# Kernel tuning notes

Measured on AMD Instinct MI355X. Metric: run time of the kernel, lower is better.

## Reference

```python
import jax, jax.numpy as jnp
import numpy as np

QUERY_DIM = 1024
KEY_DIM = 768
NUM_HEADS = 16
HEAD_DIM = QUERY_DIM // NUM_HEADS
SCALE = HEAD_DIM ** -0.5


def setup_inputs() -> dict:
    key = jax.random.key(0)
    ks = jax.random.split(key, 11)
    B, Nq, Nk = 4, 4096, 1024
    s_q = QUERY_DIM ** -0.5
    s_k = KEY_DIM ** -0.5
    return {
        "query": jax.random.normal(ks[0], (B, Nq, QUERY_DIM), jnp.float32),
        "key": jax.random.normal(ks[1], (B, Nk, KEY_DIM), jnp.float32),
        "value": jax.random.normal(ks[2], (B, Nk, KEY_DIM), jnp.float32),
        "Wq": jax.random.normal(ks[3], (QUERY_DIM, QUERY_DIM), jnp.float32) * s_q,
        "bq": jnp.zeros((QUERY_DIM,), jnp.float32),
        "Wk": jax.random.normal(ks[4], (KEY_DIM, QUERY_DIM), jnp.float32) * s_k,
        "bk": jnp.zeros((QUERY_DIM,), jnp.float32),
        "Wv": jax.random.normal(ks[5], (KEY_DIM, QUERY_DIM), jnp.float32) * s_k,
        "bv": jnp.zeros((QUERY_DIM,), jnp.float32),
        "Wo": jax.random.normal(ks[6], (QUERY_DIM, QUERY_DIM), jnp.float32) * s_q,
        "bo": jnp.zeros((QUERY_DIM,), jnp.float32),
    }


def reference(query, key, value, Wq, bq, Wk, bk, Wv, bv, Wo, bo):
    B, Nq, _ = query.shape
    Nk = key.shape[1]
    # projections to (B, H, N, d)
    q = (query @ Wq + bq).reshape(B, Nq, NUM_HEADS, HEAD_DIM).transpose(0, 2, 1, 3)
    k = (key @ Wk + bk).reshape(B, Nk, NUM_HEADS, HEAD_DIM).transpose(0, 2, 1, 3)
    v = (value @ Wv + bv).reshape(B, Nk, NUM_HEADS, HEAD_DIM).transpose(0, 2, 1, 3)
    attn = jnp.einsum("bhqd,bhkd->bhqk", q, k) * SCALE
    attn = jax.nn.softmax(attn, axis=-1)
    out = jnp.einsum("bhqk,bhkd->bhqd", attn, v)
    out = out.transpose(0, 2, 1, 3).reshape(B, Nq, QUERY_DIM)
    return out @ Wo + bo
```

## Files before the change

kernel.cpp:

```cpp
#include <hip/hip_runtime.h>
#include <hip/hip_bf16.h>
#include <stdint.h>


typedef unsigned short u16;
typedef __attribute__((ext_vector_type(8))) short short8;
typedef __attribute__((ext_vector_type(4))) float f32x4;

#define B_SZ 4
#define NQ   4096
#define NK   1024
#define QDIM 1024
#define KDIM 768
#define NH   16
#define HD   64
#define QSCALE (0.125f * 1.44269504f)

__device__ __forceinline__ u16 f2bf(float f) {
  union { float f; uint32_t u; } v; v.f = f;
  uint32_t u = v.u;
  return (u16)((u + 0x7FFFu + ((u >> 16) & 1u)) >> 16);
}

__device__ __forceinline__ uint32_t pk2(float a, float b) {
  union { __hip_bfloat162 h; uint32_t u; } cv;
  cv.h = __float22bfloat162_rn(float2{a, b});
  return cv.u;
}

__device__ __forceinline__ float fexp2(float x) {
  return __builtin_amdgcn_exp2f(x);
}

__device__ __forceinline__ void async16(u16* lds, const u16* g) {
  __builtin_amdgcn_global_load_lds(
      (__attribute__((address_space(1))) void*)(g),
      (__attribute__((address_space(3))) void*)(lds), 16, 0, 0);
}

__global__ __launch_bounds__(256) void f32_to_bf16_all(const float* __restrict__ q,
                                                       const float* __restrict__ k,
                                                       const float* __restrict__ v,
                                                       u16* __restrict__ oq,
                                                       u16* __restrict__ ok,
                                                       u16* __restrict__ ov,
                                                       int n4q, int n4kv) {
  int i = blockIdx.x * 256 + threadIdx.x;
  const float* in; u16* out; int idx;
  if (i < n4q) { in = q; out = oq; idx = i; }
  else if (i < n4q + n4kv) { in = k; out = ok; idx = i - n4q; }
  else if (i < n4q + 2 * n4kv) { in = v; out = ov; idx = i - n4q - n4kv; }
  else return;
  f32x4 vv = ((const f32x4*)in)[idx];
  uint2 o = {pk2(vv.x, vv.y), pk2(vv.z, vv.w)};
  ((uint2*)out)[idx] = o;
}

__global__ __launch_bounds__(256) void transpose4_k(const float* __restrict__ W0,
                                                    const float* __restrict__ W1,
                                                    const float* __restrict__ W2,
                                                    const float* __restrict__ W3,
                                                    u16* __restrict__ T0,
                                                    u16* __restrict__ T1,
                                                    u16* __restrict__ T2,
                                                    u16* __restrict__ T3) {
  const int z = blockIdx.z;
  const float* W = (z == 0) ? W0 : (z == 1) ? W1 : (z == 2) ? W2 : W3;
  u16* T = (z == 0) ? T0 : (z == 1) ? T1 : (z == 2) ? T2 : T3;
  const int K = (z == 1 || z == 2) ? KDIM : QDIM;
  const int N = QDIM;
  int nb = blockIdx.x * 32, kb = blockIdx.y * 32;
  if (kb >= K) return;
  __shared__ float t[32][33];
  int tx = threadIdx.x & 31, ty = threadIdx.x >> 5;
#pragma unroll
  for (int i = 0; i < 4; ++i)
    t[ty + i * 8][tx] = W[(size_t)(kb + ty + i * 8) * N + nb + tx];
  __syncthreads();
#pragma unroll
  for (int i = 0; i < 4; ++i)
    T[(size_t)(nb + ty + i * 8) * K + kb + tx] = f2bf(t[tx][ty + i * 8]);
}

__global__ __launch_bounds__(512, 2) void gemm_bt256(const u16* __restrict__ A,
                                                     const u16* __restrict__ Bt,
                                                     const float* __restrict__ bias,
                                                     float* __restrict__ Cf,
                                                     u16* __restrict__ Cb,
                                                     int M, int N, int K,
                                                     int out_bf16, float scale) {
  __shared__ __align__(16) u16 Al[3][128 * 64];
  __shared__ __align__(16) u16 Bl[3][256 * 64];
  const int tid = threadIdx.x;
  const int w = tid >> 6, lane = tid & 63;
  const int g = lane >> 4, l15 = lane & 15;
  const int sw = l15 & 7;
  const int bid = blockIdx.x;
  const int cpx = gridDim.x >> 3;
  const int swz = (bid & 7) * cpx + (bid >> 3);
  const int nby = N >> 8;
  const int mbase = (swz / nby) * 128, nbase = (swz % nby) * 256;
  const int wm = (w & 1) * 64, wn = (w >> 1) * 64;
  const int NT = K >> 6;

  const int ca0 = 0 * 512 + tid, ca1 = 1 * 512 + tid;
  const int ra0 = ca0 >> 3, rc0 = ((ca0 & 7) ^ (ra0 & 7)) * 8;
  const int ra1 = ca1 >> 3, rc1 = ((ca1 & 7) ^ (ra1 & 7)) * 8;
  const u16* pa0 = A + (size_t)(mbase + ra0) * K + rc0;
  const u16* pa1 = A + (size_t)(mbase + ra1) * K + rc1;
  const u16* pb[4];
#pragma unroll
  for (int i = 0; i < 4; ++i) {
    int c = i * 512 + tid;
    int row = c >> 3, col = ((c & 7) ^ (row & 7)) * 8;
    pb[i] = Bt + (size_t)(nbase + row) * K + col;
  }
  const int lA0 = (0 * 512 + w * 64) * 8, lA1 = (1 * 512 + w * 64) * 8;
  int lB[4];
#pragma unroll
  for (int i = 0; i < 4; ++i) lB[i] = (i * 512 + w * 64) * 8;

  f32x4 zero4 = {0.f, 0.f, 0.f, 0.f};
  f32x4 acc[4][4];
#pragma unroll
  for (int i = 0; i < 4; ++i)
#pragma unroll
    for (int j = 0; j < 4; ++j) acc[i][j] = zero4;

  async16(&Al[0][lA0], pa0); async16(&Al[0][lA1], pa1);
#pragma unroll
  for (int i = 0; i < 4; ++i) async16(&Bl[0][lB[i]], pb[i]);
  pa0 += 64; pa1 += 64;
#pragma unroll
  for (int i = 0; i < 4; ++i) pb[i] += 64;
  async16(&Al[1][lA0], pa0); async16(&Al[1][lA1], pa1);
#pragma unroll
  for (int i = 0; i < 4; ++i) async16(&Bl[1][lB[i]], pb[i]);
  pa0 += 64; pa1 += 64;
#pragma unroll
  for (int i = 0; i < 4; ++i) pb[i] += 64;
  asm volatile("s_waitcnt vmcnt(6)" ::: "memory");
  __builtin_amdgcn_sched_barrier(0);
  __builtin_amdgcn_s_barrier();

  int cb = 0, sb = 2;
  for (int kt = 0; kt < NT; ++kt) {
    const u16* Ap = &Al[cb][0];
    const u16* Bp = &Bl[cb][0];
    const bool st = (kt + 2 < NT);

    short8 af[4][2], bfa[2][2];
#pragma unroll
    for (int mt = 0; mt < 4; ++mt) {
      af[mt][0] = *(const short8*)&Ap[(wm + mt * 16 + l15) * 64 + (g ^ sw) * 8];
      af[mt][1] = *(const short8*)&Ap[(wm + mt * 16 + l15) * 64 + ((4 + g) ^ sw) * 8];
    }
#pragma unroll
    for (int nt = 0; nt < 2; ++nt) {
      bfa[nt][0] = *(const short8*)&Bp[(wn + nt * 16 + l15) * 64 + (g ^ sw) * 8];
      bfa[nt][1] = *(const short8*)&Bp[(wn + nt * 16 + l15) * 64 + ((4 + g) ^ sw) * 8];
    }
    if (st) {
      async16(&Al[sb][lA0], pa0);
      async16(&Al[sb][lA1], pa1);
      async16(&Bl[sb][lB[0]], pb[0]);
      async16(&Bl[sb][lB[1]], pb[1]);
    }
    __builtin_amdgcn_s_barrier();
    asm volatile("s_waitcnt lgkmcnt(0)" ::: "memory");
    __builtin_amdgcn_sched_barrier(0);
    __builtin_amdgcn_s_setprio(1);
#pragma unroll
    for (int ks = 0; ks < 2; ++ks)
#pragma unroll
      for (int mt = 0; mt < 4; ++mt)
#pragma unroll
        for (int nt = 0; nt < 2; ++nt)
          acc[mt][nt] = __builtin_amdgcn_mfma_f32_16x16x32_bf16(af[mt][ks], bfa[nt][ks],
                                                                acc[mt][nt], 0, 0, 0);
    __builtin_amdgcn_s_setprio(0);
    __builtin_amdgcn_s_barrier();

    short8 bfb[2][2];
#pragma unroll
    for (int nt = 0; nt < 2; ++nt) {
      bfb[nt][0] = *(const short8*)&Bp[(wn + (nt + 2) * 16 + l15) * 64 + (g ^ sw) * 8];
      bfb[nt][1] = *(const short8*)&Bp[(wn + (nt + 2) * 16 + l15) * 64 + ((4 + g) ^ sw) * 8];
    }
    if (st) {
      async16(&Bl[sb][lB[2]], pb[2]);
      async16(&Bl[sb][lB[3]], pb[3]);
      pa0 += 64; pa1 += 64;
#pragma unroll
      for (int i = 0; i < 4; ++i) pb[i] += 64;
    }
    __builtin_amdgcn_s_barrier();
    asm volatile("s_waitcnt lgkmcnt(0)" ::: "memory");
    __builtin_amdgcn_sched_barrier(0);
    __builtin_amdgcn_s_setprio(1);
#pragma unroll
    for (int ks = 0; ks < 2; ++ks)
#pragma unroll
      for (int mt = 0; mt < 4; ++mt)
#pragma unroll
        for (int nt = 0; nt < 2; ++nt)
          acc[mt][nt + 2] = __builtin_amdgcn_mfma_f32_16x16x32_bf16(af[mt][ks], bfb[nt][ks],
                                                                    acc[mt][nt + 2], 0, 0, 0);
    __builtin_amdgcn_s_setprio(0);

    if (kt < NT - 2) {
      asm volatile("s_waitcnt vmcnt(6)" ::: "memory");
    } else if (kt == NT - 2) {
      asm volatile("s_waitcnt vmcnt(0)" ::: "memory");
    }
    __builtin_amdgcn_sched_barrier(0);
    __builtin_amdgcn_s_barrier();
    cb = (cb == 2) ? 0 : cb + 1;
    sb = (sb == 2) ? 0 : sb + 1;
  }

#pragma unroll
  for (int nt = 0; nt < 4; ++nt) {
    int col = nbase + wn + nt * 16 + l15;
    float bv = bias[col];
#pragma unroll
    for (int mt = 0; mt < 4; ++mt)
#pragma unroll
      for (int r = 0; r < 4; ++r) {
        int row = mbase + wm + mt * 16 + g * 4 + r;
        float v = (acc[mt][nt][r] + bv) * scale;
        if (out_bf16) Cb[(size_t)row * N + col] = f2bf(v);
        else          Cf[(size_t)row * N + col] = v;
      }
  }
}

__global__ __launch_bounds__(256) void gemm_kv(const u16* __restrict__ kA,
                                               const u16* __restrict__ vA,
                                               const u16* __restrict__ Wk,
                                               const u16* __restrict__ Wv,
                                               const float* __restrict__ bk,
                                               const float* __restrict__ bv,
                                               u16* __restrict__ Kp,
                                               u16* __restrict__ VT,
                                               int M, int N, int K) {
  __shared__ __align__(16) u16 Al[128 * 64];
  __shared__ __align__(16) u16 Bl[128 * 64];
  const int bid = blockIdx.x;
  const int swz = (bid & 7) * 64 + (bid >> 3);
  const int ct = swz >> 8;
  const int mbase = (swz & 31) * 128, nbase = ((swz >> 5) & 7) * 128;
  const u16* A  = ct ? vA : kA;
  const u16* Bt = ct ? Wv : Wk;
  const float* bias = ct ? bv : bk;
  const int tid = threadIdx.x;
  const int w = tid >> 6, lane = tid & 63;
  const int g = lane >> 4, l15 = lane & 15;
  const int sw = l15 & 7;
  const int wm = (w & 1) * 64, wn = (w >> 1) * 64;

  f32x4 zero4 = {0.f, 0.f, 0.f, 0.f};
  f32x4 acc[4][4];
#pragma unroll
  for (int i = 0; i < 4; ++i)
#pragma unroll
    for (int j = 0; j < 4; ++j) acc[i][j] = zero4;

  for (int kb = 0; kb < K; kb += 64) {
#pragma unroll
    for (int i = 0; i < 4; ++i) {
      int cbase = w * 256 + i * 64;
      int c = cbase + lane;
      int row = c >> 3;
      int kc8 = ((c & 7) ^ (row & 7)) * 8;
      async16(&Al[cbase * 8], A + (size_t)(mbase + row) * K + kb + kc8);
      async16(&Bl[cbase * 8], Bt + (size_t)(nbase + row) * K + kb + kc8);
    }
    __syncthreads();
#pragma unroll
    for (int ks = 0; ks < 2; ++ks) {
      short8 af[4], bf[4];
#pragma unroll
      for (int mt = 0; mt < 4; ++mt)
        af[mt] = *(const short8*)&Al[(wm + mt * 16 + l15) * 64 + ((ks * 4 + g) ^ sw) * 8];
#pragma unroll
      for (int nt = 0; nt < 4; ++nt)
        bf[nt] = *(const short8*)&Bl[(wn + nt * 16 + l15) * 64 + ((ks * 4 + g) ^ sw) * 8];
      if (ct) {
#pragma unroll
        for (int nt = 0; nt < 4; ++nt)
#pragma unroll
          for (int mt = 0; mt < 4; ++mt)
            acc[nt][mt] = __builtin_amdgcn_mfma_f32_16x16x32_bf16(bf[nt], af[mt],
                                                                  acc[nt][mt], 0, 0, 0);
      } else {
#pragma unroll
        for (int mt = 0; mt < 4; ++mt)
#pragma unroll
          for (int nt = 0; nt < 4; ++nt)
            acc[mt][nt] = __builtin_amdgcn_mfma_f32_16x16x32_bf16(af[mt], bf[nt],
                                                                  acc[mt][nt], 0, 0, 0);
      }
    }
    __syncthreads();
  }

  if (ct) {
#pragma unroll
    for (int mt = 0; mt < 4; ++mt) {
      int m = mbase + wm + mt * 16 + l15;
#pragma unroll
      for (int nt = 0; nt < 4; ++nt)
#pragma unroll
        for (int r = 0; r < 4; ++r) {
          int n = nbase + wn + nt * 16 + g * 4 + r;
          VT[(size_t)n * M + m] = f2bf(acc[nt][mt][r] + bias[n]);
        }
    }
  } else {
#pragma unroll
    for (int nt = 0; nt < 4; ++nt) {
      int col = nbase + wn + nt * 16 + l15;
      float bvv = bias[col];
#pragma unroll
      for (int mt = 0; mt < 4; ++mt)
#pragma unroll
        for (int r = 0; r < 4; ++r) {
          int row = mbase + wm + mt * 16 + g * 4 + r;
          Kp[(size_t)row * N + col] = f2bf(acc[mt][nt][r] + bvv);
        }
    }
  }
}

__global__ __launch_bounds__(256, 2) void attn_kernel(const u16* __restrict__ Qp,
                                                      const u16* __restrict__ Kp,
                                                      const u16* __restrict__ VT,
                                                      u16* __restrict__ AO) {
  __shared__ __align__(16) u16 K_lds[2][64 * 64];
  __shared__ __align__(16) u16 V_lds[3][64 * 64];
  __shared__ __align__(16) u16 P_lds[4][32 * 64];

  const int tid = threadIdx.x;
  const int w = tid >> 6, lane = tid & 63;
  const int g = lane >> 4, l15 = lane & 15;
  const int sw = l15 & 7;
  const int bh = blockIdx.y, b = bh >> 4, h = bh & 15;
  const int qrow0 = blockIdx.x * 128 + w * 32;
  const int MT = B_SZ * NK;

  const int cbase0 = (w * 2 + 0) * 64;
  const int cbase1 = (w * 2 + 1) * 64;
  const int c0 = cbase0 + lane, c1 = cbase1 + lane;
  const int row0 = c0 >> 3, kc80 = ((c0 & 7) ^ (row0 & 7)) * 8;
  const int row1 = c1 >> 3, kc81 = ((c1 & 7) ^ (row1 & 7)) * 8;

  const u16* kp0 = Kp + (size_t)(b * NK + row0) * QDIM + h * HD + kc80;
  const u16* kp1 = Kp + (size_t)(b * NK + row1) * QDIM + h * HD + kc81;
  const u16* vp0 = VT + (size_t)(h * HD + row0) * MT + b * NK + kc80;
  const u16* vp1 = VT + (size_t)(h * HD + row1) * MT + b * NK + kc81;

  const int rb = l15 * 64;
  const int cs0 = (g ^ sw) * 8;
  const int cs1 = ((4 + g) ^ sw) * 8;
  const int pwb = rb + (((g >> 1) ^ (sw & 1)) * 8) + (g & 1) * 4;
  const int pms = sw & 6;

  short8 ones8;
#pragma unroll
  for (int j = 0; j < 8; ++j) ones8[j] = (short)0x3F80;

  short8 qf[2][2];
#pragma unroll
  for (int qt = 0; qt < 2; ++qt)
#pragma unroll
    for (int ks = 0; ks < 2; ++ks) {
      size_t row = (size_t)(b * NQ + qrow0 + qt * 16 + l15);
      qf[qt][ks] = *(const short8*)(Qp + row * QDIM + h * HD + ks * 32 + g * 8);
    }

  f32x4 zero4 = {0.f, 0.f, 0.f, 0.f};
  f32x4 o4[4][2];
  f32x4 lacc[2];
#pragma unroll
  for (int dt = 0; dt < 4; ++dt)
#pragma unroll
    for (int qt = 0; qt < 2; ++qt) o4[dt][qt] = zero4;
  lacc[0] = zero4; lacc[1] = zero4;

  u16* Pl = &P_lds[w][0];

  async16(&K_lds[0][cbase0 * 8], kp0);
  async16(&K_lds[0][cbase1 * 8], kp1);
  async16(&V_lds[0][cbase0 * 8], vp0);
  async16(&V_lds[0][cbase1 * 8], vp1);
  kp0 += 64 * QDIM; kp1 += 64 * QDIM; vp0 += 64; vp1 += 64;
  __syncthreads();

  async16(&K_lds[1][cbase0 * 8], kp0);
  async16(&K_lds[1][cbase1 * 8], kp1);
  async16(&V_lds[1][cbase0 * 8], vp0);
  async16(&V_lds[1][cbase1 * 8], vp1);
  kp0 += 64 * QDIM; kp1 += 64 * QDIM; vp0 += 64; vp1 += 64;

  {
    const u16* Kl = &K_lds[0][0];
    f32x4 sc[4][2];
    short8 kf0[4], kf1[4];
#pragma unroll
    for (int mt = 0; mt < 4; ++mt) {
      kf0[mt] = *(const short8*)&Kl[mt * 1024 + rb + cs0];
      kf1[mt] = *(const short8*)&Kl[mt * 1024 + rb + cs1];
    }
    __builtin_amdgcn_s_setprio(1);
#pragma unroll
    for (int mt = 0; mt < 4; ++mt)
#pragma unroll
      for (int qt = 0; qt < 2; ++qt)
        sc[mt][qt] = __builtin_amdgcn_mfma_f32_16x16x32_bf16(kf0[mt], qf[qt][0],
                                                             zero4, 0, 0, 0);
#pragma unroll
    for (int mt = 0; mt < 4; ++mt)
#pragma unroll
      for (int qt = 0; qt < 2; ++qt)
        sc[mt][qt] = __builtin_amdgcn_mfma_f32_16x16x32_bf16(kf1[mt], qf[qt][1],
                                                             sc[mt][qt], 0, 0, 0);
    __builtin_amdgcn_s_setprio(0);
#pragma unroll
    for (int qt = 0; qt < 2; ++qt)
#pragma unroll
      for (int mt = 0; mt < 4; ++mt) {
        float p0 = fexp2(sc[mt][qt][0]);
        float p1 = fexp2(sc[mt][qt][1]);
        float p2 = fexp2(sc[mt][qt][2]);
        float p3 = fexp2(sc[mt][qt][3]);
        uint2 pk = {pk2(p0, p1), pk2(p2, p3)};
        *(uint2*)&Pl[qt * 1024 + pwb + ((mt * 2) ^ pms) * 8] = pk;
      }
  }
  __syncthreads();

  for (int kc = 1; kc < NK / 64; ++kc) {
    const int pv = (kc - 1) % 3;
    if (kc + 1 < NK / 64) {
      const int nk = (kc + 1) & 1, nv = (kc + 1) % 3;
      async16(&K_lds[nk][cbase0 * 8], kp0);
      async16(&K_lds[nk][cbase1 * 8], kp1);
      async16(&V_lds[nv][cbase0 * 8], vp0);
      async16(&V_lds[nv][cbase1 * 8], vp1);
      kp0 += 64 * QDIM; kp1 += 64 * QDIM; vp0 += 64; vp1 += 64;
    }
    const u16* Kl = &K_lds[kc & 1][0];
    const u16* Vl = &V_lds[pv][0];

    short8 pb[2][2], vf[2][4], kf[2][4];
#pragma unroll
    for (int qt = 0; qt < 2; ++qt) {
      pb[0][qt] = *(const short8*)&Pl[qt * 1024 + rb + cs0];
      pb[1][qt] = *(const short8*)&Pl[qt * 1024 + rb + cs1];
    }
#pragma unroll
    for (int dt = 0; dt < 4; ++dt) {
      vf[0][dt] = *(const short8*)&Vl[dt * 1024 + rb + cs0];
      vf[1][dt] = *(const short8*)&Vl[dt * 1024 + rb + cs1];
    }
#pragma unroll
    for (int mt = 0; mt < 4; ++mt) {
      kf[0][mt] = *(const short8*)&Kl[mt * 1024 + rb + cs0];
      kf[1][mt] = *(const short8*)&Kl[mt * 1024 + rb + cs1];
    }

    f32x4 sc[4][2];
    __builtin_amdgcn_s_setprio(1);
#pragma unroll
    for (int mt = 0; mt < 4; ++mt)
#pragma unroll
      for (int qt = 0; qt < 2; ++qt)
        sc[mt][qt] = __builtin_amdgcn_mfma_f32_16x16x32_bf16(kf[0][mt], qf[qt][0],
                                                             zero4, 0, 0, 0);
#pragma unroll
    for (int qt = 0; qt < 2; ++qt)
      lacc[qt] = __builtin_amdgcn_mfma_f32_16x16x32_bf16(ones8, pb[0][qt],
                                                         lacc[qt], 0, 0, 0);
#pragma unroll
    for (int dt = 0; dt < 4; ++dt)
#pragma unroll
      for (int qt = 0; qt < 2; ++qt)
        o4[dt][qt] = __builtin_amdgcn_mfma_f32_16x16x32_bf16(vf[0][dt], pb[0][qt],
                                                             o4[dt][qt], 0, 0, 0);
#pragma unroll
    for (int mt = 0; mt < 4; ++mt)
#pragma unroll
      for (int qt = 0; qt < 2; ++qt)
        sc[mt][qt] = __builtin_amdgcn_mfma_f32_16x16x32_bf16(kf[1][mt], qf[qt][1],
                                                             sc[mt][qt], 0, 0, 0);
#pragma unroll
    for (int qt = 0; qt < 2; ++qt)
      lacc[qt] = __builtin_amdgcn_mfma_f32_16x16x32_bf16(ones8, pb[1][qt],
                                                         lacc[qt], 0, 0, 0);
#pragma unroll
    for (int dt = 0; dt < 4; ++dt)
#pragma unroll
      for (int qt = 0; qt < 2; ++qt)
        o4[dt][qt] = __builtin_amdgcn_mfma_f32_16x16x32_bf16(vf[1][dt], pb[1][qt],
                                                             o4[dt][qt], 0, 0, 0);
    __builtin_amdgcn_s_setprio(0);

#pragma unroll
    for (int qt = 0; qt < 2; ++qt)
#pragma unroll
      for (int mt = 0; mt < 4; ++mt) {
        float p0 = fexp2(sc[mt][qt][0]);
        float p1 = fexp2(sc[mt][qt][1]);
        float p2 = fexp2(sc[mt][qt][2]);
        float p3 = fexp2(sc[mt][qt][3]);
        uint2 pk = {pk2(p0, p1), pk2(p2, p3)};
        *(uint2*)&Pl[qt * 1024 + pwb + ((mt * 2) ^ pms) * 8] = pk;
      }

    asm volatile("s_waitcnt vmcnt(2)" ::: "memory");
    __builtin_amdgcn_sched_barrier(0);
    __builtin_amdgcn_s_barrier();
  }

  asm volatile("s_waitcnt vmcnt(0)" ::: "memory");
  __builtin_amdgcn_sched_barrier(0);
  __builtin_amdgcn_s_barrier();

  {
    const u16* Vl = &V_lds[(NK / 64 - 1) % 3][0];
    short8 pb[2][2], vf[2][4];
#pragma unroll
    for (int qt = 0; qt < 2; ++qt) {
      pb[0][qt] = *(const short8*)&Pl[qt * 1024 + rb + cs0];
      pb[1][qt] = *(const short8*)&Pl[qt * 1024 + rb + cs1];
    }
#pragma unroll
    for (int dt = 0; dt < 4; ++dt) {
      vf[0][dt] = *(const short8*)&Vl[dt * 1024 + rb + cs0];
      vf[1][dt] = *(const short8*)&Vl[dt * 1024 + rb + cs1];
    }
    __builtin_amdgcn_s_setprio(1);
#pragma unroll
    for (int ks = 0; ks < 2; ++ks) {
#pragma unroll
      for (int qt = 0; qt < 2; ++qt)
        lacc[qt] = __builtin_amdgcn_mfma_f32_16x16x32_bf16(ones8, pb[ks][qt],
                                                           lacc[qt], 0, 0, 0);
#pragma unroll
      for (int dt = 0; dt < 4; ++dt)
#pragma unroll
        for (int qt = 0; qt < 2; ++qt)
          o4[dt][qt] = __builtin_amdgcn_mfma_f32_16x16x32_bf16(vf[ks][dt], pb[ks][qt],
                                                               o4[dt][qt], 0, 0, 0);
    }
    __builtin_amdgcn_s_setprio(0);
  }

#pragma unroll
  for (int qt = 0; qt < 2; ++qt) {
    float inv = __builtin_amdgcn_rcpf(lacc[qt][0]);
    size_t row = (size_t)(b * NQ + qrow0 + qt * 16 + l15);
#pragma unroll
    for (int dt = 0; dt < 4; ++dt) {
      uint2 pk = {pk2(o4[dt][qt][0] * inv, o4[dt][qt][1] * inv),
                  pk2(o4[dt][qt][2] * inv, o4[dt][qt][3] * inv)};
      *(uint2*)(AO + row * QDIM + h * HD + dt * 16 + g * 4) = pk;
    }
  }
}

extern "C" void kernel_launch(void* const* d_in, const int* in_sizes, int n_in,
                              void* d_out, int out_size, void* d_ws, size_t ws_size,
                              hipStream_t stream) {
  const float* query = (const float*)d_in[0];
  const float* key   = (const float*)d_in[1];
  const float* value = (const float*)d_in[2];
  const float* Wq = (const float*)d_in[3];
  const float* bq = (const float*)d_in[4];
  const float* Wk = (const float*)d_in[5];
  const float* bk = (const float*)d_in[6];
  const float* Wv = (const float*)d_in[7];
  const float* bv = (const float*)d_in[8];
  const float* Wo = (const float*)d_in[9];
  const float* bo = (const float*)d_in[10];

  char* ws = (char*)d_ws;
  size_t off = 0;
  auto alloc = [&](size_t bytes) -> void* {
    void* p = ws + off;
    off += (bytes + 255) & ~(size_t)255;
    return p;
  };
  const size_t NQTOT = (size_t)B_SZ * NQ;
  const size_t NKTOT = (size_t)B_SZ * NK;
  u16* qbf = (u16*)alloc(NQTOT * QDIM * 2);
  u16* kbf = (u16*)alloc(NKTOT * KDIM * 2);
  u16* vbf = (u16*)alloc(NKTOT * KDIM * 2);
  u16* wqt = (u16*)alloc((size_t)QDIM * QDIM * 2);
  u16* wkt = (u16*)alloc((size_t)KDIM * QDIM * 2);
  u16* wvt = (u16*)alloc((size_t)KDIM * QDIM * 2);
  u16* wot = (u16*)alloc((size_t)QDIM * QDIM * 2);
  u16* Qp  = (u16*)alloc(NQTOT * QDIM * 2);
  u16* Kp  = (u16*)alloc(NKTOT * QDIM * 2);
  u16* VT  = (u16*)alloc((size_t)QDIM * NKTOT * 2);
  u16* AO  = qbf;

  {
    int n4q  = (int)(NQTOT * QDIM / 4);
    int n4kv = (int)(NKTOT * KDIM / 4);
    int nb = (n4q + 2 * n4kv + 255) / 256;
    f32_to_bf16_all<<<nb, 256, 0, stream>>>(query, key, value, qbf, kbf, vbf,
                                            n4q, n4kv);
  }
  transpose4_k<<<dim3(QDIM / 32, QDIM / 32, 4), 256, 0, stream>>>(
      Wq, Wk, Wv, Wo, wqt, wkt, wvt, wot);

  gemm_bt256<<<(NQTOT / 128) * (QDIM / 256), 512, 0, stream>>>(
      qbf, wqt, bq, nullptr, Qp, (int)NQTOT, QDIM, QDIM, 1, QSCALE);
  gemm_kv<<<(NKTOT / 128) * (QDIM / 128) * 2, 256, 0, stream>>>(
      kbf, vbf, wkt, wvt, bk, bv, Kp, VT, (int)NKTOT, QDIM, KDIM);

  attn_kernel<<<dim3(NQ / 128, B_SZ * NH), 256, 0, stream>>>(Qp, Kp, VT, AO);

  gemm_bt256<<<(NQTOT / 128) * (QDIM / 256), 512, 0, stream>>>(
      AO, wot, bo, (float*)d_out, nullptr, (int)NQTOT, QDIM, QDIM, 0, 1.0f);

  (void)in_sizes; (void)n_in; (void)out_size; (void)ws_size;
}
```

Baseline: 392.1 us.

## Keep softmax P in registers via permlane swaps, drop P LDS, swizzle grid

The exponentiated score tile is converted into the MFMA B-operand layout in registers using v_permlane32/16_swap, so the per-wave P shared-memory buffer and its store/load round trip go away. Dropping that buffer cuts LDS use, and launch bounds rise to 4 blocks per CU for higher occupancy. The grid becomes 1D with a block-index swizzle that changes which (batch,head) tiles run together, aiming at better K/V cache reuse. The end-of-loop barrier is now a plain __syncthreads skipped on the last iteration, which risks register pressure or spills at the higher occupancy target.

```diff
diff --git a/kernel.cpp b/kernel.cpp
--- a/kernel.cpp
+++ b/kernel.cpp
@@ -333,21 +333,24 @@
   }
 }
 
-__global__ __launch_bounds__(256, 2) void attn_kernel(const u16* __restrict__ Qp,
+__global__ __launch_bounds__(256, 4) void attn_kernel(const u16* __restrict__ Qp,
                                                       const u16* __restrict__ Kp,
                                                       const u16* __restrict__ VT,
                                                       u16* __restrict__ AO) {
   __shared__ __align__(16) u16 K_lds[2][64 * 64];
   __shared__ __align__(16) u16 V_lds[3][64 * 64];
-  __shared__ __align__(16) u16 P_lds[4][32 * 64];
 
   const int tid = threadIdx.x;
   const int w = tid >> 6, lane = tid & 63;
   const int g = lane >> 4, l15 = lane & 15;
   const int sw = l15 & 7;
-  const int bh = blockIdx.y, b = bh >> 4, h = bh & 15;
-  const int qrow0 = blockIdx.x * 128 + w * 32;
+  const int bid = blockIdx.x;
+  const int swzb = (bid & 7) * 256 + (bid >> 3);
+  const int bh = swzb >> 5, qblk = swzb & 31;
+  const int b = bh >> 4, h = bh & 15;
+  const int qrow0 = qblk * 128 + w * 32;
   const int MT = B_SZ * NK;
+  const int NT4 = NK / 64;
 
   const int cbase0 = (w * 2 + 0) * 64;
   const int cbase1 = (w * 2 + 1) * 64;
@@ -363,8 +366,6 @@
   const int rb = l15 * 64;
   const int cs0 = (g ^ sw) * 8;
   const int cs1 = ((4 + g) ^ sw) * 8;
-  const int pwb = rb + (((g >> 1) ^ (sw & 1)) * 8) + (g & 1) * 4;
-  const int pms = sw & 6;
 
   short8 ones8;
 #pragma unroll
@@ -388,7 +389,26 @@
     for (int qt = 0; qt < 2; ++qt) o4[dt][qt] = zero4;
   lacc[0] = zero4; lacc[1] = zero4;
 
-  u16* Pl = &P_lds[w][0];
+  short8 pr[2][2];
+
+  auto packP = [&](const f32x4 (&sc)[4][2], short8 (&prr)[2][2]) {
+#pragma unroll
+    for (int qt = 0; qt < 2; ++qt)
+#pragma unroll
+      for (int ks = 0; ks < 2; ++ks) {
+        uint32_t A0 = pk2(fexp2(sc[2 * ks][qt][0]), fexp2(sc[2 * ks][qt][1]));
+        uint32_t A1 = pk2(fexp2(sc[2 * ks][qt][2]), fexp2(sc[2 * ks][qt][3]));
+        uint32_t B0 = pk2(fexp2(sc[2 * ks + 1][qt][0]), fexp2(sc[2 * ks + 1][qt][1]));
+        uint32_t B1 = pk2(fexp2(sc[2 * ks + 1][qt][2]), fexp2(sc[2 * ks + 1][qt][3]));
+        asm volatile("v_permlane32_swap_b32 %0, %1" : "+v"(A0), "+v"(B0));
+        asm volatile("v_permlane32_swap_b32 %0, %1" : "+v"(A1), "+v"(B1));
+        asm volatile("v_permlane16_swap_b32 %0, %1" : "+v"(A0), "+v"(B0));
+        asm volatile("v_permlane16_swap_b32 %0, %1" : "+v"(A1), "+v"(B1));
+        union { uint32_t u[4]; short8 s; } wd;
+        wd.u[0] = A0; wd.u[1] = A1; wd.u[2] = B0; wd.u[3] = B1;
+        prr[ks][qt] = wd.s;
+      }
+  };
 
   async16(&K_lds[0][cbase0 * 8], kp0);
   async16(&K_lds[0][cbase1 * 8], kp1);
@@ -426,23 +446,12 @@
         sc[mt][qt] = __builtin_amdgcn_mfma_f32_16x16x32_bf16(kf1[mt], qf[qt][1],
                                                              sc[mt][qt], 0, 0, 0);
     __builtin_amdgcn_s_setprio(0);
-#pragma unroll
-    for (int qt = 0; qt < 2; ++qt)
-#pragma unroll
-      for (int mt = 0; mt < 4; ++mt) {
-        float p0 = fexp2(sc[mt][qt][0]);
-        float p1 = fexp2(sc[mt][qt][1]);
-        float p2 = fexp2(sc[mt][qt][2]);
-        float p3 = fexp2(sc[mt][qt][3]);
-        uint2 pk = {pk2(p0, p1), pk2(p2, p3)};
-        *(uint2*)&Pl[qt * 1024 + pwb + ((mt * 2) ^ pms) * 8] = pk;
-      }
+    packP(sc, pr);
   }
   __syncthreads();
 
-  for (int kc = 1; kc < NK / 64; ++kc) {
-    const int pv = (kc - 1) % 3;
-    if (kc + 1 < NK / 64) {
+  for (int kc = 1; kc < NT4; ++kc) {
+    if (kc + 1 < NT4) {
       const int nk = (kc + 1) & 1, nv = (kc + 1) % 3;
       async16(&K_lds[nk][cbase0 * 8], kp0);
       async16(&K_lds[nk][cbase1 * 8], kp1);
@@ -451,14 +460,9 @@
       kp0 += 64 * QDIM; kp1 += 64 * QDIM; vp0 += 64; vp1 += 64;
     }
     const u16* Kl = &K_lds[kc & 1][0];
-    const u16* Vl = &V_lds[pv][0];
-
-    short8 pb[2][2], vf[2][4], kf[2][4];
-#pragma unroll
-    for (int qt = 0; qt < 2; ++qt) {
-      pb[0][qt] = *(const short8*)&Pl[qt * 1024 + rb + cs0];
-      pb[1][qt] = *(const short8*)&Pl[qt * 1024 + rb + cs1];
-    }
+    const u16* Vl = &V_lds[(kc - 1) % 3][0];
+
+    short8 vf[2][4], kf[2][4];
 #pragma unroll
     for (int dt = 0; dt < 4; ++dt) {
       vf[0][dt] = *(const short8*)&Vl[dt * 1024 + rb + cs0];
@@ -480,13 +484,13 @@
                                                              zero4, 0, 0, 0);
 #pragma unroll
     for (int qt = 0; qt < 2; ++qt)
-      lacc[qt] = __builtin_amdgcn_mfma_f32_16x16x32_bf16(ones8, pb[0][qt],
+      lacc[qt] = __builtin_amdgcn_mfma_f32_16x16x32_bf16(ones8, pr[0][qt],
                                                          lacc[qt], 0, 0, 0);
 #pragma unroll
     for (int dt = 0; dt < 4; ++dt)
 #pragma unroll
       for (int qt = 0; qt < 2; ++qt)
-        o4[dt][qt] = __builtin_amdgcn_mfma_f32_16x16x32_bf16(vf[0][dt], pb[0][qt],
+        o4[dt][qt] = __builtin_amdgcn_mfma_f32_16x16x32_bf16(vf[0][dt], pr[0][qt],
                                                              o4[dt][qt], 0, 0, 0);
 #pragma unroll
     for (int mt = 0; mt < 4; ++mt)
@@ -496,45 +500,24 @@
                                                              sc[mt][qt], 0, 0, 0);
 #pragma unroll
     for (int qt = 0; qt < 2; ++qt)
-      lacc[qt] = __builtin_amdgcn_mfma_f32_16x16x32_bf16(ones8, pb[1][qt],
+      lacc[qt] = __builtin_amdgcn_mfma_f32_16x16x32_bf16(ones8, pr[1][qt],
                                                          lacc[qt], 0, 0, 0);
 #pragma unroll
     for (int dt = 0; dt < 4; ++dt)
 #pragma unroll
       for (int qt = 0; qt < 2; ++qt)
-        o4[dt][qt] = __builtin_amdgcn_mfma_f32_16x16x32_bf16(vf[1][dt], pb[1][qt],
+        o4[dt][qt] = __builtin_amdgcn_mfma_f32_16x16x32_bf16(vf[1][dt], pr[1][qt],
                                                              o4[dt][qt], 0, 0, 0);
     __builtin_amdgcn_s_setprio(0);
 
-#pragma unroll
-    for (int qt = 0; qt < 2; ++qt)
-#pragma unroll
-      for (int mt = 0; mt < 4; ++mt) {
-        float p0 = fexp2(sc[mt][qt][0]);
-        float p1 = fexp2(sc[mt][qt][1]);
-        float p2 = fexp2(sc[mt][qt][2]);
-        float p3 = fexp2(sc[mt][qt][3]);
-        uint2 pk = {pk2(p0, p1), pk2(p2, p3)};
-        *(uint2*)&Pl[qt * 1024 + pwb + ((mt * 2) ^ pms) * 8] = pk;
-      }
-
-    asm volatile("s_waitcnt vmcnt(2)" ::: "memory");
-    __builtin_amdgcn_sched_barrier(0);
-    __builtin_amdgcn_s_barrier();
-  }
-
-  asm volatile("s_waitcnt vmcnt(0)" ::: "memory");
-  __builtin_amdgcn_sched_barrier(0);
-  __builtin_amdgcn_s_barrier();
+    packP(sc, pr);
+
+    if (kc + 1 < NT4) __syncthreads();
+  }
 
   {
-    const u16* Vl = &V_lds[(NK / 64 - 1) % 3][0];
-    short8 pb[2][2], vf[2][4];
-#pragma unroll
-    for (int qt = 0; qt < 2; ++qt) {
-      pb[0][qt] = *(const short8*)&Pl[qt * 1024 + rb + cs0];
-      pb[1][qt] = *(const short8*)&Pl[qt * 1024 + rb + cs1];
-    }
+    const u16* Vl = &V_lds[(NT4 - 1) % 3][0];
+    short8 vf[2][4];
 #pragma unroll
     for (int dt = 0; dt < 4; ++dt) {
       vf[0][dt] = *(const short8*)&Vl[dt * 1024 + rb + cs0];
@@ -545,13 +528,13 @@
     for (int ks = 0; ks < 2; ++ks) {
 #pragma unroll
       for (int qt = 0; qt < 2; ++qt)
-        lacc[qt] = __builtin_amdgcn_mfma_f32_16x16x32_bf16(ones8, pb[ks][qt],
+        lacc[qt] = __builtin_amdgcn_mfma_f32_16x16x32_bf16(ones8, pr[ks][qt],
                                                            lacc[qt], 0, 0, 0);
 #pragma unroll
       for (int dt = 0; dt < 4; ++dt)
 #pragma unroll
         for (int qt = 0; qt < 2; ++qt)
-          o4[dt][qt] = __builtin_amdgcn_mfma_f32_16x16x32_bf16(vf[ks][dt], pb[ks][qt],
+          o4[dt][qt] = __builtin_amdgcn_mfma_f32_16x16x32_bf16(vf[ks][dt], pr[ks][qt],
                                                                o4[dt][qt], 0, 0, 0);
     }
     __builtin_amdgcn_s_setprio(0);
@@ -621,7 +604,7 @@
   gemm_kv<<<(NKTOT / 128) * (QDIM / 128) * 2, 256, 0, stream>>>(
       kbf, vbf, wkt, wvt, bk, bv, Kp, VT, (int)NKTOT, QDIM, KDIM);
 
-  attn_kernel<<<dim3(NQ / 128, B_SZ * NH), 256, 0, stream>>>(Qp, Kp, VT, AO);
+  attn_kernel<<<(NQ / 128) * (B_SZ * NH), 256, 0, stream>>>(Qp, Kp, VT, AO);
 
   gemm_bt256<<<(NQTOT / 128) * (QDIM / 256), 512, 0, stream>>>(
       AO, wot, bo, (float*)d_out, nullptr, (int)NQTOT, QDIM, QDIM, 0, 1.0f);
```

Result: slower. 563.0 us (+43.6%).
